# Kernel optimization log

Measured on AMD Instinct MI355X. Metric: run time of the kernel, lower is better.

The kernel has to match this reference:

```python
import jax, jax.numpy as jnp
import numpy as np

DIMS = [1024, 2048, 2048, 51]
B, P = 16, 1024


def setup_inputs() -> dict:
    key = jax.random.key(0)
    ks = jax.random.split(key, 1 + 2 * (len(DIMS) - 1))
    inp = {
        "num_pairs": P,
        "classifier_input": jax.random.normal(ks[0], (B, P, DIMS[0]), dtype=jnp.float32),
        "num_batches": B,
    }
    # Linear params, PyTorch-style: W[out, in], b[out]
    for li in range(len(DIMS) - 1):
        fan_in = DIMS[li]
        bound = 1.0 / np.sqrt(fan_in)
        inp[f"W{li}"] = jax.random.uniform(ks[1 + 2 * li], (DIMS[li + 1], fan_in), minval=-bound, maxval=bound, dtype=jnp.float32)
        inp[f"b{li}"] = jax.random.uniform(ks[2 + 2 * li], (DIMS[li + 1],), minval=-bound, maxval=bound, dtype=jnp.float32)
    return inp


def reference(num_pairs, classifier_input, num_batches, W0, b0, W1, b1, W2, b2):
    # Batched MLP over all (num_batches * num_pairs) vectors at once.
    # Original loops per (b, i); math is identical. dropout p=0.0 -> identity.
    x = classifier_input  # [B, P, d_in]
    x = jax.nn.relu(jnp.einsum("bpd,hd->bph", x, W0) + b0)
    x = jax.nn.relu(jnp.einsum("bpd,hd->bph", x, W1) + b1)
    out = jnp.einsum("bpd,od->bpo", x, W2) + b2  # [B, P, n_classes]
    return out
```

## Files before the change

### kernel.cpp

```cpp
#include <hip/hip_runtime.h>
#include <hip/hip_bf16.h>
#include <stdint.h>

typedef __attribute__((ext_vector_type(8))) short short8;
typedef __attribute__((ext_vector_type(8))) uint16_t ushort8;
typedef __attribute__((ext_vector_type(4))) float floatx4;

#define TK 64


__device__ __forceinline__ uint16_t f2bf_bits(float f) {
    uint32_t u = __builtin_bit_cast(uint32_t, f);
    u += 0x7FFFu + ((u >> 16) & 1u);
    return (uint16_t)(u >> 16);
}

__device__ __forceinline__ void async_copy16(const void* g, void* l) {
    auto gp = (const __attribute__((address_space(1))) uint32_t*)(uintptr_t)g;
    auto lp = (__attribute__((address_space(3))) uint32_t*)(uint32_t)(uintptr_t)l;
    __builtin_amdgcn_global_load_lds(gp, lp, 16, 0, 0);
}


__global__ void cvt8(const float* __restrict__ src, uint16_t* __restrict__ dst, int n) {
    int i = (blockIdx.x * 256 + threadIdx.x) * 8;
    if (i >= n) return;
    floatx4 a = *(const floatx4*)(src + i);
    floatx4 b = *(const floatx4*)(src + i + 4);
    ushort8 o;
#pragma unroll
    for (int k = 0; k < 4; k++) {
        o[k]     = f2bf_bits(a[k]);
        o[k + 4] = f2bf_bits(b[k]);
    }
    *(ushort8*)(dst + i) = o;
}

__global__ void cvt_pad_w2(const float* __restrict__ src, uint16_t* __restrict__ dst) {
    int i = (blockIdx.x * 256 + threadIdx.x) * 8;
    int row = i >> 11;
    ushort8 o;
    if (row < 51) {
        floatx4 a = *(const floatx4*)(src + i);
        floatx4 b = *(const floatx4*)(src + i + 4);
#pragma unroll
        for (int k = 0; k < 4; k++) {
            o[k]     = f2bf_bits(a[k]);
            o[k + 4] = f2bf_bits(b[k]);
        }
    } else {
#pragma unroll
        for (int k = 0; k < 8; k++) o[k] = 0;
    }
    *(ushort8*)(dst + i) = o;
}


template <int MI, int NJ, bool RELU, bool OUTF32>
__global__ __launch_bounds__(256, 2)
void gemm_bt(const uint16_t* __restrict__ A,
             const uint16_t* __restrict__ W,
             const float* __restrict__ bias,
             void* __restrict__ out,
             int M, int N, int K, int ldc, int nstore)
{
    constexpr int TMv = MI * 32;
    constexpr int TNv = NJ * 32;
    constexpr int ACH = TMv / 32;
    constexpr int BCH = TNv / 32;

    __shared__ alignas(16) uint16_t sA[TMv * TK];
    __shared__ alignas(16) uint16_t sB[TNv * TK];

    const int tid  = threadIdx.x;
    const int wave = tid >> 6;
    const int lane = tid & 63;

    const int f   = blockIdx.x;
    const int xcd = f & 7;
    const int loc = f >> 3;
    const int per = (int)gridDim.x >> 3;
    const int nt  = N / TNv;
    const int n_t = loc % nt;
    const int m_t = xcd * (per / nt) + loc / nt;
    const int n0 = n_t * TNv;
    const int m0 = m_t * TMv;

    floatx4 acc[MI][NJ];
    const floatx4 zero = {0.f, 0.f, 0.f, 0.f};
#pragma unroll
    for (int i = 0; i < MI; i++)
#pragma unroll
        for (int j = 0; j < NJ; j++) acc[i][j] = zero;

    const int wr = (wave >> 1) * MI * 16;
    const int wc = (wave & 1) * NJ * 16;

    const int sr   = lane >> 3;
    const int scol = ((lane & 7) ^ sr) * 8;

    const uint16_t* ap[ACH];
    const uint16_t* bp[BCH];
#pragma unroll
    for (int t = 0; t < ACH; t++)
        ap[t] = A + (size_t)(m0 + (wave + 4 * t) * 8 + sr) * K + scol;
#pragma unroll
    for (int t = 0; t < BCH; t++)
        bp[t] = W + (size_t)(n0 + (wave + 4 * t) * 8 + sr) * K + scol;

    const int fm = lane & 15;
    const int fr = fm & 7;
    const int kgb = lane >> 4;

    const int niter = K / TK;
    for (int it = 0; it < niter; it++) {
#pragma unroll
        for (int t = 0; t < ACH; t++) {
            async_copy16(ap[t], sA + (wave + 4 * t) * 512);
            ap[t] += TK;
        }
#pragma unroll
        for (int t = 0; t < BCH; t++) {
            async_copy16(bp[t], sB + (wave + 4 * t) * 512);
            bp[t] += TK;
        }
        __syncthreads();

#pragma unroll
        for (int kk = 0; kk < 2; kk++) {
            const int slot = ((kgb + 4 * kk) ^ fr) * 8;
            short8 af[MI], bfr[NJ];
#pragma unroll
            for (int i = 0; i < MI; i++)
                af[i] = *(const short8*)(sA + (wr + i * 16 + fm) * TK + slot);
#pragma unroll
            for (int j = 0; j < NJ; j++)
                bfr[j] = *(const short8*)(sB + (wc + j * 16 + fm) * TK + slot);
#pragma unroll
            for (int i = 0; i < MI; i++)
#pragma unroll
                for (int j = 0; j < NJ; j++)
                    acc[i][j] = __builtin_amdgcn_mfma_f32_16x16x32_bf16(af[i], bfr[j], acc[i][j], 0, 0, 0);
        }
        __syncthreads();
    }

    const int cr = (lane >> 4) * 4;
    const int cc = lane & 15;
#pragma unroll
    for (int i = 0; i < MI; i++) {
        const int gmb = m0 + wr + i * 16 + cr;
#pragma unroll
        for (int j = 0; j < NJ; j++) {
            const int gn = n0 + wc + j * 16 + cc;
            if (gn < nstore) {
                const float bv = bias[gn];
#pragma unroll
                for (int r = 0; r < 4; r++) {
                    float v = acc[i][j][r] + bv;
                    if (RELU) v = fmaxf(v, 0.f);
                    const size_t idx = (size_t)(gmb + r) * ldc + gn;
                    if (OUTF32) ((float*)out)[idx] = v;
                    else        ((uint16_t*)out)[idx] = f2bf_bits(v);
                }
            }
        }
    }
}


#define SCHED0 __builtin_amdgcn_sched_barrier(0)

#define LOAD_AF(SA, QM, DST) do { \
    const uint16_t* _p = (SA) + (QM) * 8192 + aoff; \
    _Pragma("unroll") \
    for (int kk = 0; kk < 2; kk++) { \
      const int sl = ((kgb + 4 * kk) ^ fr) * 8; \
      _Pragma("unroll") \
      for (int mi = 0; mi < 4; mi++) \
        DST[mi][kk] = *(const short8*)(_p + mi * 1024 + sl); \
    } } while (0)

#define LOAD_BF(SB, QN, BF) do { \
    const uint16_t* _p = (SB) + (QN) * 8192 + boff; \
    _Pragma("unroll") \
    for (int kk = 0; kk < 2; kk++) { \
      const int sl = ((kgb + 4 * kk) ^ fr) * 8; \
      _Pragma("unroll") \
      for (int nj = 0; nj < 2; nj++) \
        BF[nj][kk] = *(const short8*)(_p + nj * 1024 + sl); \
    } } while (0)

#define PH_SYNC \
    SCHED0; \
    asm volatile("s_waitcnt lgkmcnt(0)" ::: "memory"); \
    SCHED0; \
    __builtin_amdgcn_s_barrier(); \
    SCHED0;

#define PH_SYNC_VM \
    SCHED0; \
    asm volatile("s_waitcnt vmcnt(0) lgkmcnt(0)" ::: "memory"); \
    SCHED0; \
    __builtin_amdgcn_s_barrier(); \
    SCHED0;

#define MFMA_CL(QM, QN, AF, BF) \
    __builtin_amdgcn_s_setprio(1); \
    _Pragma("unroll") \
    for (int kk = 0; kk < 2; kk++) \
      _Pragma("unroll") \
      for (int mi = 0; mi < 4; mi++) \
        _Pragma("unroll") \
        for (int nj = 0; nj < 2; nj++) \
          acc[QM][QN][mi][nj] = __builtin_amdgcn_mfma_f32_16x16x32_bf16( \
              AF[mi][kk], BF[nj][kk], acc[QM][QN][mi][nj], 0, 0, 0); \
    __builtin_amdgcn_s_setprio(0); \
    SCHED0;

#define TILE_BODY(SAc, SBc, SAo, SBo, TT, STG) \
     \
    if (STG) { stB((TT) + 1, SBo); stA((TT) + 1, SAo); } \
    LOAD_AF(SAc, 0, af); \
    LOAD_BF(SBc, 0, b0); \
    LOAD_BF(SBc, 1, b1); \
    PH_SYNC; \
    MFMA_CL(0, 0, af, b0); \
    MFMA_CL(0, 1, af, b1); \
     \
    LOAD_AF(SAc, 1, af); \
    PH_SYNC_VM; \
    MFMA_CL(1, 0, af, b0); \
    MFMA_CL(1, 1, af, b1);

template <bool RELU, bool OUTF32>
__global__ __launch_bounds__(512, 2)
void gemm256(const uint16_t* __restrict__ A,
             const uint16_t* __restrict__ W,
             const float* __restrict__ bias,
             void* __restrict__ out,
             int K, int N, int ldc, int nstore)
{
    extern __shared__ uint16_t smem[];
    uint16_t* sA0 = smem;
    uint16_t* sA1 = smem + 16384;
    uint16_t* sB0 = smem + 32768;
    uint16_t* sB1 = smem + 49152;

    const int tid  = threadIdx.x;
    const int wave = tid >> 6;
    const int lane = tid & 63;
    const int wm2  = wave >> 2;
    const int wn2  = wave & 3;

    const int f   = blockIdx.x;
    const int xcd = f & 7;
    const int loc = f >> 3;
    const int per = (int)gridDim.x >> 3;
    const int ntn = N / 256;
    const int n_t = loc % ntn;
    const int m_t = xcd * (per / ntn) + loc / ntn;
    const int m0 = m_t * 256;
    const int n0 = n_t * 256;

    floatx4 acc[2][2][4][2];
    const floatx4 zero = {0.f, 0.f, 0.f, 0.f};
#pragma unroll
    for (int qm = 0; qm < 2; qm++)
#pragma unroll
    for (int qn = 0; qn < 2; qn++)
#pragma unroll
    for (int mi = 0; mi < 4; mi++)
#pragma unroll
    for (int nj = 0; nj < 2; nj++) acc[qm][qn][mi][nj] = zero;

    const int srow = lane >> 3;
    const int scol = ((lane & 7) ^ srow) * 8;
    const uint16_t* pA = A + (size_t)(m0 + wave * 8 + srow) * K + scol;
    const uint16_t* pB = W + (size_t)(n0 + wave * 8 + srow) * K + scol;

    auto stA = [&](int kt, uint16_t* buf) {
        const uint16_t* p = pA + (size_t)kt * 64;
        async_copy16(p,                    buf + wave * 512);
        async_copy16(p + (size_t)64  * K,  buf + 4096  + wave * 512);
        async_copy16(p + (size_t)128 * K,  buf + 8192  + wave * 512);
        async_copy16(p + (size_t)192 * K,  buf + 12288 + wave * 512);
    };
    auto stB = [&](int kt, uint16_t* buf) {
        const uint16_t* p = pB + (size_t)kt * 64;
        async_copy16(p,                    buf + wave * 512);
        async_copy16(p + (size_t)64  * K,  buf + 4096  + wave * 512);
        async_copy16(p + (size_t)128 * K,  buf + 8192  + wave * 512);
        async_copy16(p + (size_t)192 * K,  buf + 12288 + wave * 512);
    };

    const int fm  = lane & 15;
    const int fr  = fm & 7;
    const int kgb = lane >> 4;
    const int aoff = (wm2 * 64 + fm) * 64;
    const int boff = (wn2 * 32 + fm) * 64;

    short8 af[4][2];
    short8 b0[2][2];
    short8 b1[2][2];

    stB(0, sB0);
    stA(0, sA0);
    asm volatile("s_waitcnt vmcnt(0)" ::: "memory");
    __builtin_amdgcn_s_barrier();
    SCHED0;

    const int niter = K / 64;
    for (int it = 0; it < niter / 2 - 1; ++it) {
        TILE_BODY(sA0, sB0, sA1, sB1, 2 * it,     true);
        TILE_BODY(sA1, sB1, sA0, sB0, 2 * it + 1, true);
    }
    TILE_BODY(sA0, sB0, sA1, sB1, niter - 2, true);
    TILE_BODY(sA1, sB1, sA0, sB0, niter - 1, false);

    const int cr = (lane >> 4) * 4;
    const int cc = lane & 15;
#pragma unroll
    for (int qm = 0; qm < 2; qm++)
#pragma unroll
    for (int mi = 0; mi < 4; mi++) {
        const int gm = m0 + qm * 128 + wm2 * 64 + mi * 16 + cr;
#pragma unroll
        for (int qn = 0; qn < 2; qn++)
#pragma unroll
        for (int nj = 0; nj < 2; nj++) {
            const int gn = n0 + qn * 128 + wn2 * 32 + nj * 16 + cc;
            if (gn < nstore) {
                const float bv = bias[gn];
#pragma unroll
                for (int r = 0; r < 4; r++) {
                    float v = acc[qm][qn][mi][nj][r] + bv;
                    if (RELU) v = fmaxf(v, 0.f);
                    const size_t idx = (size_t)(gm + r) * ldc + gn;
                    if (OUTF32) ((float*)out)[idx] = v;
                    else        ((uint16_t*)out)[idx] = f2bf_bits(v);
                }
            }
        }
    }
}


extern "C" void kernel_launch(void* const* d_in, const int* in_sizes, int n_in,
                              void* d_out, int out_size, void* d_ws, size_t ws_size,
                              hipStream_t stream) {
    (void)in_sizes; (void)n_in; (void)out_size; (void)ws_size;
    const float* X  = (const float*)d_in[1];
    const float* W0 = (const float*)d_in[3];
    const float* b0 = (const float*)d_in[4];
    const float* W1 = (const float*)d_in[5];
    const float* b1 = (const float*)d_in[6];
    const float* W2 = (const float*)d_in[7];
    const float* b2 = (const float*)d_in[8];

    const int M = 16384;

    static bool attr_done = false;
    if (!attr_done) {
        (void)hipFuncSetAttribute((const void*)gemm256<true, false>,
                                  hipFuncAttributeMaxDynamicSharedMemorySize, 131072);
        attr_done = true;
    }

    char* w = (char*)d_ws;
    uint16_t* X0  = (uint16_t*)w; w += (size_t)M * 1024 * 2;
    uint16_t* X1  = (uint16_t*)w; w += (size_t)M * 2048 * 2;
    uint16_t* X2  = (uint16_t*)w; w += (size_t)M * 2048 * 2;
    uint16_t* W0b = (uint16_t*)w; w += (size_t)2048 * 1024 * 2;
    uint16_t* W1b = (uint16_t*)w; w += (size_t)2048 * 2048 * 2;
    uint16_t* W2b = (uint16_t*)w; w += (size_t)64 * 2048 * 2;

    cvt8<<<M * 1024 / 8 / 256, 256, 0, stream>>>(X, X0, M * 1024);
    cvt8<<<2048 * 1024 / 8 / 256, 256, 0, stream>>>(W0, W0b, 2048 * 1024);
    cvt8<<<2048 * 2048 / 8 / 256, 256, 0, stream>>>(W1, W1b, 2048 * 2048);
    cvt_pad_w2<<<64 * 2048 / 8 / 256, 256, 0, stream>>>(W2, W2b);

    gemm256<true, false><<<dim3((M / 256) * (2048 / 256)), 512, 131072, stream>>>(
        X0, W0b, b0, X1, 1024, 2048, 2048, 2048);
    gemm256<true, false><<<dim3((M / 256) * (2048 / 256)), 512, 131072, stream>>>(
        X1, W1b, b1, X2, 2048, 2048, 2048, 2048);
    gemm_bt<1, 2, false, true><<<dim3(M / 32), 256, 0, stream>>>(
        X2, W2b, b2, d_out, M, 64, 2048, 51, 51);
}
```

Measured before the change: 351.0 us.

## Ping-pong wave roles so half the waves compute while others load LDS

Splits the eight waves into two role groups by wm2 that run out of phase. One group issues LDS fragment loads while the other runs its MFMA cluster, and barriers alternate between the groups. The intent is to overlap LDS reads with matrix math across waves instead of having every wave wait at a shared load-then-compute barrier. The trade-off is more complex synchronisation; skewed waits on vmcnt and lgkmcnt could expose hazards on the shared buffers.

Result: slower. 1.056 ms (+201.0%).

```diff
diff --git a/kernel.cpp b/kernel.cpp
--- a/kernel.cpp
+++ b/kernel.cpp
@@ -170,6 +170,9 @@
 
 
 #define SCHED0 __builtin_amdgcn_sched_barrier(0)
+#define BAR    __builtin_amdgcn_s_barrier()
+#define LGKM0  asm volatile("s_waitcnt lgkmcnt(0)" ::: "memory")
+#define VM0    asm volatile("s_waitcnt vmcnt(0)" ::: "memory")
 
 #define LOAD_AF(SA, QM, DST) do { \
     const uint16_t* _p = (SA) + (QM) * 8192 + aoff; \
@@ -190,20 +193,6 @@
       for (int nj = 0; nj < 2; nj++) \
         BF[nj][kk] = *(const short8*)(_p + nj * 1024 + sl); \
     } } while (0)
-
-#define PH_SYNC \
-    SCHED0; \
-    asm volatile("s_waitcnt lgkmcnt(0)" ::: "memory"); \
-    SCHED0; \
-    __builtin_amdgcn_s_barrier(); \
-    SCHED0;
-
-#define PH_SYNC_VM \
-    SCHED0; \
-    asm volatile("s_waitcnt vmcnt(0) lgkmcnt(0)" ::: "memory"); \
-    SCHED0; \
-    __builtin_amdgcn_s_barrier(); \
-    SCHED0;
 
 #define MFMA_CL(QM, QN, AF, BF) \
     __builtin_amdgcn_s_setprio(1); \
@@ -218,20 +207,31 @@
     __builtin_amdgcn_s_setprio(0); \
     SCHED0;
 
-#define TILE_BODY(SAc, SBc, SAo, SBo, TT, STG) \
-     \
+#define WIN_A(SAc, SBc, SAo, SBo, TT, STG, FIRST) \
     if (STG) { stB((TT) + 1, SBo); stA((TT) + 1, SAo); } \
-    LOAD_AF(SAc, 0, af); \
-    LOAD_BF(SBc, 0, b0); \
-    LOAD_BF(SBc, 1, b1); \
-    PH_SYNC; \
-    MFMA_CL(0, 0, af, b0); \
-    MFMA_CL(0, 1, af, b1); \
-     \
-    LOAD_AF(SAc, 1, af); \
-    PH_SYNC_VM; \
-    MFMA_CL(1, 0, af, b0); \
-    MFMA_CL(1, 1, af, b1);
+    SCHED0; \
+    if (role) { \
+      if (!(FIRST)) { MFMA_CL(1, 0, af, b0); MFMA_CL(1, 1, af, b1); } \
+      LOAD_AF(SAc, 0, af); LOAD_BF(SBc, 0, b0); LOAD_BF(SBc, 1, b1); \
+      SCHED0; LGKM0; SCHED0; BAR; SCHED0; \
+    } else { \
+      LOAD_AF(SAc, 0, af); LOAD_BF(SBc, 0, b0); LOAD_BF(SBc, 1, b1); \
+      SCHED0; \
+      MFMA_CL(0, 0, af, b0); MFMA_CL(0, 1, af, b1); \
+      BAR; SCHED0; \
+    }
+
+#define WIN_B(SAc, TT) \
+    if (role) { \
+      MFMA_CL(0, 0, af, b0); MFMA_CL(0, 1, af, b1); \
+      LOAD_AF(SAc, 1, af); \
+      SCHED0; LGKM0; VM0; SCHED0; BAR; SCHED0; \
+    } else { \
+      LOAD_AF(SAc, 1, af); \
+      SCHED0; \
+      MFMA_CL(1, 0, af, b0); MFMA_CL(1, 1, af, b1); \
+      VM0; SCHED0; BAR; SCHED0; \
+    }
 
 template <bool RELU, bool OUTF32>
 __global__ __launch_bounds__(512, 2)
@@ -252,6 +252,7 @@
     const int lane = tid & 63;
     const int wm2  = wave >> 2;
     const int wn2  = wave & 3;
+    const int role = wm2;
 
     const int f   = blockIdx.x;
     const int xcd = f & 7;
@@ -306,17 +307,27 @@
 
     stB(0, sB0);
     stA(0, sA0);
-    asm volatile("s_waitcnt vmcnt(0)" ::: "memory");
-    __builtin_amdgcn_s_barrier();
+    VM0;
+    BAR;
     SCHED0;
 
     const int niter = K / 64;
-    for (int it = 0; it < niter / 2 - 1; ++it) {
-        TILE_BODY(sA0, sB0, sA1, sB1, 2 * it,     true);
-        TILE_BODY(sA1, sB1, sA0, sB0, 2 * it + 1, true);
-    }
-    TILE_BODY(sA0, sB0, sA1, sB1, niter - 2, true);
-    TILE_BODY(sA1, sB1, sA0, sB0, niter - 1, false);
+    WIN_A(sA0, sB0, sA1, sB1, 0, true, true);
+    WIN_B(sA0, 0);
+    WIN_A(sA1, sB1, sA0, sB0, 1, true, false);
+    WIN_B(sA1, 1);
+    for (int it = 1; it <= niter / 2 - 2; ++it) {
+        const int T = 2 * it;
+        WIN_A(sA0, sB0, sA1, sB1, T, true, false);
+        WIN_B(sA0, T);
+        WIN_A(sA1, sB1, sA0, sB0, T + 1, true, false);
+        WIN_B(sA1, T + 1);
+    }
+    WIN_A(sA0, sB0, sA1, sB1, niter - 2, true, false);
+    WIN_B(sA0, niter - 2);
+    WIN_A(sA1, sB1, sA0, sB0, niter - 1, false, false);
+    WIN_B(sA1, niter - 1);
+    if (role) { MFMA_CL(1, 0, af, b0); MFMA_CL(1, 1, af, b1); }
 
     const int cr = (lane >> 4) * 4;
     const int cc = lane & 15;
```
